# Kernel optimization log

Measured on AMD Instinct MI355X. Metric: run time of the kernel, lower is better.

## Reference

```python
import jax, jax.numpy as jnp
import numpy as np
from jax import lax

B, C, H, W = 4, 64, 256, 256
CH = C // 2  # attention hidden channels


def conv2d_same(x, w, b):
    # x: [B,Ci,H,W], w: [Co,Ci,kh,kw]
    y = lax.conv_general_dilated(x, w, (1, 1), 'SAME',
                                 dimension_numbers=('NCHW', 'OIHW', 'NCHW'))
    return y + b[None, :, None, None]


def conv1x1(x, w):
    # w: [Co,Ci]
    return jnp.einsum('oi,bihw->bohw', w, x)


def irnn_scan(x, w, b, axis, reverse):
    """Directional IRNN: h_t = relu(x_t + w_c * h_{t-1} + b_c), per channel.
    axis: 2 (rows/H) or 3 (cols/W). reverse=True scans from the far edge
    (e.g. bottom-to-top for 'up', right-to-left for 'left')."""
    xs = jnp.moveaxis(x, axis, 0)            # [L, B, C, rest]
    wb = w[None, :, None]                    # broadcast over [B, C, rest]
    bb = b[None, :, None]

    def step(h, xt):
        h = jax.nn.relu(xt + wb * h + bb)
        return h, h

    h0 = jnp.zeros_like(xs[0])
    _, ys = lax.scan(step, h0, xs, reverse=reverse)
    return jnp.moveaxis(ys, 0, axis)


def setup_inputs() -> dict:
    key = jax.random.key(0)
    ks = jax.random.split(key, 16)
    d = {}
    d['x'] = jax.random.normal(ks[0], (B, C, H, W), dtype=jnp.float32)
    # conv_in: 1x1, no bias
    d['w_in'] = jax.random.normal(ks[1], (C, C), dtype=jnp.float32) * 0.05
    # IRNN depthwise 1x1 weights (init alpha=1.0 in torch) + biases
    for i, name in enumerate(['up', 'right', 'down', 'left']):
        d['w_' + name] = jnp.ones((C,), dtype=jnp.float32)
        d['b_' + name] = jax.random.normal(ks[2 + i], (C,), dtype=jnp.float32) * 0.01
    # convD2: 1x1, 4C -> C, no bias
    d['wD2'] = jax.random.normal(ks[6], (C, 4 * C), dtype=jnp.float32) * 0.01
    # attention layers
    d['a1_w'] = jax.random.normal(ks[7], (CH, C, 3, 3), dtype=jnp.float32) * 0.05
    d['a1_b'] = jnp.zeros((CH,), dtype=jnp.float32)
    d['a2_w'] = jax.random.normal(ks[8], (CH, CH, 3, 3), dtype=jnp.float32) * 0.05
    d['a2_b'] = jnp.zeros((CH,), dtype=jnp.float32)
    d['a3_w'] = jax.random.normal(ks[9], (1, CH), dtype=jnp.float32) * 0.05
    d['a3_b'] = jnp.zeros((1,), dtype=jnp.float32)
    return d


def reference(x, w_in, w_up, b_up, w_right, b_right, w_down, b_down,
              w_left, b_left, wD2, a1_w, a1_b, a2_w, a2_b, a3_w, a3_b):
    out = conv1x1(x, w_in)
    # four directional spatial IRNN scans
    top_up = irnn_scan(out, w_up, b_up, axis=2, reverse=True)     # bottom->top
    top_right = irnn_scan(out, w_right, b_right, axis=3, reverse=False)  # left->right
    top_down = irnn_scan(out, w_down, b_down, axis=2, reverse=False)     # top->bottom
    top_left = irnn_scan(out, w_left, b_left, axis=3, reverse=True)      # right->left
    cat = jnp.concatenate([top_up, top_right, top_down, top_left], axis=1)  # [B,4C,H,W]
    out = jax.nn.relu(conv1x1(cat, wD2))
    # attention gate
    a = jax.nn.relu(conv2d_same(out, a1_w, a1_b))
    a = jax.nn.relu(conv2d_same(a, a2_w, a2_b))
    a = conv1x1(a, a3_w) + a3_b[None, :, None, None]
    weight = jax.nn.sigmoid(a)                # [B,1,H,W]
    return jax.nn.relu(x * weight)
```

## Files before the change

### kernel.cpp

```cpp
#include <hip/hip_runtime.h>
#include <hip/hip_bf16.h>

#define HWSZ  65536

typedef unsigned short ushort_t;
typedef unsigned int   uint_t;
typedef __attribute__((ext_vector_type(8))) _Float16 half8;
typedef __attribute__((ext_vector_type(2))) _Float16 half2v;
typedef __attribute__((ext_vector_type(4))) float f32x4;

static __device__ __forceinline__ void gl_lds16(const void* g, void* l) {
    __builtin_amdgcn_global_load_lds(
        (const __attribute__((address_space(1))) unsigned int*)g,
        (__attribute__((address_space(3))) unsigned int*)l, 16, 0, 0);
}

__global__ __launch_bounds__(256) void k1_mfma(
    const float* __restrict__ x, const float* __restrict__ w_in,
    _Float16* __restrict__ out0)
{
    __shared__ float xs[64][64];
    __shared__ _Float16 ah[64][72];
    __shared__ _Float16 al[64][72];
    int b   = blockIdx.x >> 10;
    int hw0 = (blockIdx.x & 1023) << 6;
    const float* xb = x + ((size_t)b * 64) * HWSZ + hw0;
    int wave = threadIdx.x >> 6, lane = threadIdx.x & 63;
    int n16 = lane & 15, quad = lane >> 4;

    for (int idx = threadIdx.x; idx < 1024; idx += 256) {
        int i = idx >> 4, p4 = (idx & 15) << 2;
        *(float4*)&xs[i][p4] = *(const float4*)(xb + (size_t)i * HWSZ + p4);
    }

    half8 Bh[2], Bl[2];
#pragma unroll
    for (int s = 0; s < 2; s++) {
        const float* wp = w_in + (wave * 16 + n16) * 64 + s * 32 + quad * 8;
#pragma unroll
        for (int j = 0; j < 8; j++) {
            float v = wp[j];
            _Float16 h = (_Float16)v;
            float r = v - (float)h;
            Bh[s][j] = h; Bl[s][j] = (_Float16)r;
        }
    }
    __syncthreads();

    {
        int px  = threadIdx.x & 63;
        int ic0 = (threadIdx.x >> 6) << 4;
        half8 h0, h1, l0, l1;
#pragma unroll
        for (int e = 0; e < 8; e++) {
            float v = xs[ic0 + e][px];
            _Float16 h = (_Float16)v;
            h0[e] = h; l0[e] = (_Float16)(v - (float)h);
        }
#pragma unroll
        for (int e = 0; e < 8; e++) {
            float v = xs[ic0 + 8 + e][px];
            _Float16 h = (_Float16)v;
            h1[e] = h; l1[e] = (_Float16)(v - (float)h);
        }
        *(half8*)&ah[px][ic0]     = h0;
        *(half8*)&ah[px][ic0 + 8] = h1;
        *(half8*)&al[px][ic0]     = l0;
        *(half8*)&al[px][ic0 + 8] = l1;
    }
    __syncthreads();

    f32x4 acc[4] = {};
#pragma unroll
    for (int j = 0; j < 4; j++) {
        int px = j * 16 + n16;
#pragma unroll
        for (int s = 0; s < 2; s++) {
            half8 Ah = *(const half8*)&ah[px][s * 32 + quad * 8];
            half8 Al = *(const half8*)&al[px][s * 32 + quad * 8];
            acc[j] = __builtin_amdgcn_mfma_f32_16x16x32_f16(Ah, Bh[s], acc[j], 0, 0, 0);
            acc[j] = __builtin_amdgcn_mfma_f32_16x16x32_f16(Al, Bh[s], acc[j], 0, 0, 0);
            acc[j] = __builtin_amdgcn_mfma_f32_16x16x32_f16(Ah, Bl[s], acc[j], 0, 0, 0);
        }
    }
    _Float16* ob = out0 + ((size_t)b * HWSZ + hw0) * 64 + wave * 16;
#pragma unroll
    for (int j = 0; j < 4; j++)
#pragma unroll
        for (int r = 0; r < 4; r++) {
            int px = j * 16 + quad * 4 + r;
            ob[(size_t)px * 64 + n16] = (_Float16)acc[j][r];
        }
}

__global__ __launch_bounds__(256) void k2_scan(
    const _Float16* __restrict__ out0,
    const float* __restrict__ w_up, const float* __restrict__ b_up,
    const float* __restrict__ w_rt, const float* __restrict__ b_rt,
    const float* __restrict__ w_dn, const float* __restrict__ b_dn,
    const float* __restrict__ w_lf, const float* __restrict__ b_lf,
    _Float16* __restrict__ cat)
{
    int c2 = threadIdx.x & 31;
    int q  = threadIdx.x >> 5;
    int dir = blockIdx.x >> 7;
    int bid = blockIdx.x & 127;
    int b = bid >> 5, g = bid & 31;
    int line = g * 8 + q;
    size_t base = (size_t)b * HWSZ;
    bool vert = dir < 2;
    bool rev  = dir & 1;

    const float *wp, *bp; int coff;
    if      (dir == 0) { wp = w_dn; bp = b_dn; coff = 128; }
    else if (dir == 1) { wp = w_up; bp = b_up; coff = 0;   }
    else if (dir == 2) { wp = w_rt; bp = b_rt; coff = 64;  }
    else               { wp = w_lf; bp = b_lf; coff = 192; }
    float w0v = wp[2 * c2], b0v = bp[2 * c2];
    float w1v = wp[2 * c2 + 1], b1v = bp[2 * c2 + 1];
    int coff2 = coff >> 1;

    const half2v* src = (const half2v*)out0;
    half2v* dst = (half2v*)cat;

    float h0 = 0.f, h1 = 0.f;
    for (int k0 = 0; k0 < 256; k0 += 16) {
        half2v v[16];
#pragma unroll
        for (int jx = 0; jx < 16; jx++) {
            int i = rev ? 255 - (k0 + jx) : (k0 + jx);
            size_t pix = vert ? (base + i * 256 + line) : (base + line * 256 + i);
            v[jx] = src[pix * 32 + c2];
        }
#pragma unroll
        for (int jx = 0; jx < 16; jx++) {
            int i = rev ? 255 - (k0 + jx) : (k0 + jx);
            size_t pix = vert ? (base + i * 256 + line) : (base + line * 256 + i);
            h0 = fmaxf(0.f, (float)v[jx][0] + w0v * h0 + b0v);
            h1 = fmaxf(0.f, (float)v[jx][1] + w1v * h1 + b1v);
            half2v o; o[0] = (_Float16)h0; o[1] = (_Float16)h1;
            dst[pix * 128 + coff2 + c2] = o;
        }
    }
}

__global__ __launch_bounds__(256) void packall(
    const float* __restrict__ wD2, const float* __restrict__ a1w,
    const float* __restrict__ a2w,
    _Float16* __restrict__ wf, _Float16* __restrict__ p1,
    _Float16* __restrict__ p2)
{
    int i = blockIdx.x * 256 + threadIdx.x;
    if (i < 16384) {
        wf[i] = (_Float16)wD2[i];
        return;
    }
    int k = i - 16384;
    if (k < 18432) {
        int j = k & 7, lane = (k >> 3) & 63, st = k >> 9;
        int s = st >> 1, t = st & 1;
        int oc = t * 16 + (lane & 15);
        int gk = s * 32 + (lane >> 4) * 8 + j;
        int dydx = gk >> 6, ic = gk & 63;
        p1[k] = (_Float16)a1w[((oc * 64 + ic) * 3 + dydx / 3) * 3 + dydx % 3];
    } else if (k < 27648) {
        int e = k - 18432;
        int j = e & 7, lane = (e >> 3) & 63, st = e >> 9;
        int s = st >> 1, t = st & 1;
        int oc = t * 16 + (lane & 15);
        int gk = s * 32 + (lane >> 4) * 8 + j;
        int dydx = gk >> 5, ic = gk & 31;
        p2[e] = (_Float16)a2w[((oc * 32 + ic) * 3 + dydx / 3) * 3 + dydx % 3];
    }
}

__global__ __launch_bounds__(256) void k3_mfma(
    const _Float16* __restrict__ cat, const _Float16* __restrict__ wf,
    _Float16* __restrict__ out3)
{
    __shared__ _Float16 As[64 * 256];
    int wave = threadIdx.x >> 6, lane = threadIdx.x & 63;
    int n16 = lane & 15, quad = lane >> 4;
    size_t p0 = (size_t)blockIdx.x * 64;

    half8 B[8];
#pragma unroll
    for (int s = 0; s < 8; s++)
        B[s] = *(const half8*)(wf + (size_t)(wave * 16 + n16) * 256 + s * 32 + quad * 8);

#pragma unroll
    for (int it = 0; it < 8; it++) {
        int px = wave * 16 + it * 2 + (lane >> 5);
        int pu = lane & 31;
        int lu = pu ^ (px & 7);
        const _Float16* gp = cat + ((p0 + px) << 8) + lu * 8;
        _Float16* lp = As + wave * 4096 + it * 512;
        gl_lds16(gp, lp);
    }
    __syncthreads();

    f32x4 acc[4] = {};
#pragma unroll
    for (int j = 0; j < 4; j++) {
        int px = j * 16 + n16;
        const _Float16* lrow = As + px * 256;
        int x7 = px & 7;
#pragma unroll
        for (int s = 0; s < 8; s++) {
            int phys = (s * 4 + quad) ^ x7;
            half8 a = *(const half8*)(lrow + phys * 8);
            acc[j] = __builtin_amdgcn_mfma_f32_16x16x32_f16(a, B[s], acc[j], 0, 0, 0);
        }
    }

#pragma unroll
    for (int j = 0; j < 4; j++)
#pragma unroll
        for (int r = 0; r < 4; r++) {
            size_t op = (p0 + j * 16 + quad * 4 + r) * 64 + wave * 16 + n16;
            out3[op] = (_Float16)fmaxf(acc[j][r], 0.f);
        }
}

template <int IC>
__global__ __launch_bounds__(256) void convmfma(
    const _Float16* __restrict__ in, const _Float16* __restrict__ pb,
    const float* __restrict__ bias, _Float16* __restrict__ oh)
{
    constexpr int UPX = IC / 8;
    constexpr int KST = IC / 32;
    constexpr int PPS = 64 / UPX;
    __shared__ _Float16 Ls[6 * 66 * IC];

    int wave = threadIdx.x >> 6, lane = threadIdx.x & 63;
    int n16 = lane & 15, quad = lane >> 4;
    int bid = blockIdx.x;
    int bb  = bid >> 8;
    int hh0 = ((bid >> 2) & 63) << 2;
    int w0  = (bid & 3) << 6;
    const _Float16* ib = in + (size_t)bb * HWSZ * IC;

#pragma unroll
    for (int it = 0; it < (6 * UPX) / 4; it++) {
        int q   = it * 4 + wave;
        int r   = q / UPX, seg = q % UPX;
        int gh  = hh0 - 1 + r;
        int pxr = seg * PPS + lane / UPX;
        int pu  = lane % UPX;
        int px_lin = r * 66 + 1 + pxr;
        int lu  = (UPX == 8) ? (pu ^ (px_lin & 7)) : pu;
        _Float16* lp = Ls + (size_t)(r * 66 + 1 + seg * PPS) * IC;
        if ((unsigned)gh < 256u) {
            const _Float16* gp = ib + ((size_t)(gh * 256 + w0 + pxr)) * IC + lu * 8;
            gl_lds16(gp, lp);
        } else {
            half8 z = {};
            *(half8*)(lp + (size_t)lane * 8) = z;
        }
    }
    if (threadIdx.x < 12 * UPX) {
        int pu = threadIdx.x % UPX;
        int ph = threadIdx.x / UPX;
        int r = ph >> 1, side = ph & 1;
        int col = side ? 65 : 0;
        int gh = hh0 - 1 + r;
        int gw = w0 - 1 + side * 65;
        int px_lin = r * 66 + col;
        int lu = (UPX == 8) ? (pu ^ (px_lin & 7)) : pu;
        half8 v = {};
        if ((unsigned)gh < 256u && (unsigned)gw < 256u)
            v = *(const half8*)(ib + ((size_t)(gh * 256 + gw)) * IC + lu * 8);
        *(half8*)(Ls + (size_t)px_lin * IC + pu * 8) = v;
    }
    __syncthreads();

    f32x4 acc[4][2] = {};
#pragma unroll
    for (int dydx = 0; dydx < 9; dydx++) {
        int dy = dydx / 3, dx = dydx % 3;
        int r_lds = wave + dy;
#pragma unroll
        for (int kst = 0; kst < KST; kst++) {
            int s = dydx * KST + kst;
            half8 B0 = *(const half8*)(pb + (size_t)((s * 2 + 0) * 64 + lane) * 8);
            half8 B1 = *(const half8*)(pb + (size_t)((s * 2 + 1) * 64 + lane) * 8);
            int u = kst * 4 + quad;
#pragma unroll
            for (int j = 0; j < 4; j++) {
                int px_lin = r_lds * 66 + j * 16 + n16 + dx;
                int phys = (UPX == 8) ? (u ^ (px_lin & 7)) : u;
                half8 A = *(const half8*)(Ls + (size_t)px_lin * IC + phys * 8);
                acc[j][0] = __builtin_amdgcn_mfma_f32_16x16x32_f16(A, B0, acc[j][0], 0, 0, 0);
                acc[j][1] = __builtin_amdgcn_mfma_f32_16x16x32_f16(A, B1, acc[j][1], 0, 0, 0);
            }
        }
    }

    int hh = hh0 + wave;
#pragma unroll
    for (int t = 0; t < 2; t++) {
        float bv = bias[t * 16 + n16];
#pragma unroll
        for (int j = 0; j < 4; j++)
#pragma unroll
            for (int r = 0; r < 4; r++) {
                int wp = w0 + j * 16 + quad * 4 + r;
                size_t op = ((size_t)bb * HWSZ + hh * 256 + wp) * 32 + t * 16 + n16;
                oh[op] = (_Float16)fmaxf(acc[j][t][r] + bv, 0.f);
            }
    }
}

__global__ __launch_bounds__(256) void k6g(
    const _Float16* __restrict__ a2, const float* __restrict__ a3w,
    const float* __restrict__ a3b, float* __restrict__ gbuf)
{
    int pix = blockIdx.x * 256 + threadIdx.x;
    const _Float16* ap = a2 + (size_t)pix * 32;
    half8 q0 = *(const half8*)(ap);
    half8 q1 = *(const half8*)(ap + 8);
    half8 q2 = *(const half8*)(ap + 16);
    half8 q3 = *(const half8*)(ap + 24);
    float s = a3b[0];
#pragma unroll
    for (int j = 0; j < 8; j++) {
        s += a3w[j]      * (float)q0[j];
        s += a3w[j + 8]  * (float)q1[j];
        s += a3w[j + 16] * (float)q2[j];
        s += a3w[j + 24] * (float)q3[j];
    }
    gbuf[pix] = 1.f / (1.f + __expf(-s));
}

__global__ __launch_bounds__(256) void k6b(
    const float* __restrict__ x, const float* __restrict__ gbuf,
    float* __restrict__ out)
{
    const float4* x4 = (const float4*)x;
    const float4* g4 = (const float4*)gbuf;
    float4* o4 = (float4*)out;
    size_t base = (size_t)blockIdx.x * 2048;
#pragma unroll
    for (int k = 0; k < 8; k++) {
        size_t e = base + k * 256 + threadIdx.x;
        int plane = (int)(e >> 14);
        int hw4   = (int)(e & 16383);
        int b     = plane >> 6;
        float4 xv = x4[e];
        float4 gv = g4[(size_t)b * 16384 + hw4];
        float4 ov;
        ov.x = fmaxf(0.f, xv.x * gv.x);
        ov.y = fmaxf(0.f, xv.y * gv.y);
        ov.z = fmaxf(0.f, xv.z * gv.z);
        ov.w = fmaxf(0.f, xv.w * gv.w);
        o4[e] = ov;
    }
}

extern "C" void kernel_launch(void* const* d_in, const int* in_sizes, int n_in,
                              void* d_out, int out_size, void* d_ws, size_t ws_size,
                              hipStream_t stream)
{
    const float* x     = (const float*)d_in[0];
    const float* w_in  = (const float*)d_in[1];
    const float* w_up  = (const float*)d_in[2];
    const float* b_up  = (const float*)d_in[3];
    const float* w_rt  = (const float*)d_in[4];
    const float* b_rt  = (const float*)d_in[5];
    const float* w_dn  = (const float*)d_in[6];
    const float* b_dn  = (const float*)d_in[7];
    const float* w_lf  = (const float*)d_in[8];
    const float* b_lf  = (const float*)d_in[9];
    const float* wD2   = (const float*)d_in[10];
    const float* a1w   = (const float*)d_in[11];
    const float* a1b   = (const float*)d_in[12];
    const float* a2w   = (const float*)d_in[13];
    const float* a2b   = (const float*)d_in[14];
    const float* a3w   = (const float*)d_in[15];
    const float* a3b   = (const float*)d_in[16];
    float* out = (float*)d_out;

    char* ws = (char*)d_ws;
    _Float16* out0 = (_Float16*)ws;
    _Float16* out3 = (_Float16*)ws;
    _Float16* wf16 = (_Float16*)(ws + (33ull << 20));
    _Float16* p1   = (_Float16*)(ws + (34ull << 20));
    _Float16* p2   = (_Float16*)(ws + (35ull << 20));
    float*    gbuf = (float*)   (ws + (36ull << 20));
    _Float16* cat  = (_Float16*)(ws + (64ull << 20));
    _Float16* a1   = (_Float16*)(ws + (64ull << 20));
    _Float16* a2   = (_Float16*)(ws + (80ull << 20));

    k1_mfma   <<<4096, 256, 0, stream>>>(x, w_in, out0);
    k2_scan   <<<512,  256, 0, stream>>>(out0, w_up, b_up, w_rt, b_rt,
                                         w_dn, b_dn, w_lf, b_lf, cat);
    packall   <<<172,  256, 0, stream>>>(wD2, a1w, a2w, wf16, p1, p2);
    k3_mfma   <<<4096, 256, 0, stream>>>(cat, wf16, out3);
    convmfma<64><<<1024, 256, 0, stream>>>(out3, p1, a1b, a1);
    convmfma<32><<<1024, 256, 0, stream>>>(a1, p2, a2b, a2);
    k6g       <<<1024, 256, 0, stream>>>(a2, a3w, a3b, gbuf);
    k6b       <<<2048, 256, 0, stream>>>(x, gbuf, out);
}
```

Baseline: 270.6 us.

## Split IRNN scans into two halves and fuse gate conv into second attention conv

The scan kernel now gives each line to two thread groups. One half runs the recurrence over the first 128 steps while the other prefetches the second 128 inputs into shared memory, then finishes the scan from the carried hidden state. This doubles the grid and shortens the serial latency chain spent on loads. Separately, the 1x1 gate projection and sigmoid are folded into the epilogue of the second 3x3 conv using cross-lane shuffles, which removes the a2 intermediate write/read and one kernel launch.

```diff
diff --git a/kernel.cpp b/kernel.cpp
--- a/kernel.cpp
+++ b/kernel.cpp
@@ -101,12 +101,15 @@
     const float* __restrict__ w_lf, const float* __restrict__ b_lf,
     _Float16* __restrict__ cat)
 {
-    int c2 = threadIdx.x & 31;
-    int q  = threadIdx.x >> 5;
-    int dir = blockIdx.x >> 7;
-    int bid = blockIdx.x & 127;
-    int b = bid >> 5, g = bid & 31;
-    int line = g * 8 + q;
+    __shared__ half2v ls[4][128][32];
+    __shared__ float hmid[4][32][2];
+    int c2   = threadIdx.x & 31;
+    int q    = (threadIdx.x >> 5) & 3;
+    int half = threadIdx.x >> 7;
+    int dir  = blockIdx.x >> 8;
+    int bid  = blockIdx.x & 255;
+    int b = bid >> 6, g = bid & 63;
+    int line = g * 4 + q;
     size_t base = (size_t)b * HWSZ;
     bool vert = dir < 2;
     bool rev  = dir & 1;
@@ -123,25 +126,52 @@
     const half2v* src = (const half2v*)out0;
     half2v* dst = (half2v*)cat;
 
-    float h0 = 0.f, h1 = 0.f;
-    for (int k0 = 0; k0 < 256; k0 += 16) {
-        half2v v[16];
-#pragma unroll
-        for (int jx = 0; jx < 16; jx++) {
-            int i = rev ? 255 - (k0 + jx) : (k0 + jx);
-            size_t pix = vert ? (base + i * 256 + line) : (base + line * 256 + i);
-            v[jx] = src[pix * 32 + c2];
-        }
-#pragma unroll
-        for (int jx = 0; jx < 16; jx++) {
-            int i = rev ? 255 - (k0 + jx) : (k0 + jx);
-            size_t pix = vert ? (base + i * 256 + line) : (base + line * 256 + i);
-            h0 = fmaxf(0.f, (float)v[jx][0] + w0v * h0 + b0v);
-            h1 = fmaxf(0.f, (float)v[jx][1] + w1v * h1 + b1v);
-            half2v o; o[0] = (_Float16)h0; o[1] = (_Float16)h1;
-            dst[pix * 128 + coff2 + c2] = o;
-        }
-    }
+#define PIXOF(k) (vert ? (base + (size_t)(rev ? 255 - (k) : (k)) * 256 + line) \
+                       : (base + line * 256 + (size_t)(rev ? 255 - (k) : (k))))
+
+    if (half == 0) {
+        float h0 = 0.f, h1 = 0.f;
+        for (int k0 = 0; k0 < 128; k0 += 16) {
+            half2v v[16];
+#pragma unroll
+            for (int jx = 0; jx < 16; jx++)
+                v[jx] = src[PIXOF(k0 + jx) * 32 + c2];
+#pragma unroll
+            for (int jx = 0; jx < 16; jx++) {
+                h0 = fmaxf(0.f, (float)v[jx][0] + w0v * h0 + b0v);
+                h1 = fmaxf(0.f, (float)v[jx][1] + w1v * h1 + b1v);
+                half2v o; o[0] = (_Float16)h0; o[1] = (_Float16)h1;
+                dst[PIXOF(k0 + jx) * 128 + coff2 + c2] = o;
+            }
+        }
+        hmid[q][c2][0] = h0; hmid[q][c2][1] = h1;
+    } else {
+        for (int k0 = 0; k0 < 128; k0 += 16) {
+            half2v v[16];
+#pragma unroll
+            for (int jx = 0; jx < 16; jx++)
+                v[jx] = src[PIXOF(128 + k0 + jx) * 32 + c2];
+#pragma unroll
+            for (int jx = 0; jx < 16; jx++)
+                ls[q][k0 + jx][c2] = v[jx];
+        }
+    }
+    __syncthreads();
+
+    if (half == 1) {
+        float h0 = hmid[q][c2][0], h1 = hmid[q][c2][1];
+        for (int k0 = 0; k0 < 128; k0 += 16) {
+#pragma unroll
+            for (int jx = 0; jx < 16; jx++) {
+                half2v v = ls[q][k0 + jx][c2];
+                h0 = fmaxf(0.f, (float)v[0] + w0v * h0 + b0v);
+                h1 = fmaxf(0.f, (float)v[1] + w1v * h1 + b1v);
+                half2v o; o[0] = (_Float16)h0; o[1] = (_Float16)h1;
+                dst[PIXOF(128 + k0 + jx) * 128 + coff2 + c2] = o;
+            }
+        }
+    }
+#undef PIXOF
 }
 
 __global__ __launch_bounds__(256) void packall(
@@ -222,10 +252,12 @@
         }
 }
 
-template <int IC>
+template <int IC, bool GATE>
 __global__ __launch_bounds__(256) void convmfma(
     const _Float16* __restrict__ in, const _Float16* __restrict__ pb,
-    const float* __restrict__ bias, _Float16* __restrict__ oh)
+    const float* __restrict__ bias, _Float16* __restrict__ oh,
+    const float* __restrict__ a3w, const float* __restrict__ a3b,
+    float* __restrict__ gbuf)
 {
     constexpr int UPX = IC / 8;
     constexpr int KST = IC / 32;
@@ -297,39 +329,40 @@
     }
 
     int hh = hh0 + wave;
-#pragma unroll
-    for (int t = 0; t < 2; t++) {
-        float bv = bias[t * 16 + n16];
+    if constexpr (GATE) {
+        float bv0 = bias[n16], bv1 = bias[16 + n16];
+        float aw0 = a3w[n16], aw1 = a3w[16 + n16];
+        float ab  = a3b[0];
 #pragma unroll
         for (int j = 0; j < 4; j++)
 #pragma unroll
             for (int r = 0; r < 4; r++) {
-                int wp = w0 + j * 16 + quad * 4 + r;
-                size_t op = ((size_t)bb * HWSZ + hh * 256 + wp) * 32 + t * 16 + n16;
-                oh[op] = (_Float16)fmaxf(acc[j][t][r] + bv, 0.f);
+                float r0 = fmaxf(acc[j][0][r] + bv0, 0.f);
+                float r1 = fmaxf(acc[j][1][r] + bv1, 0.f);
+                float sv = fmaf(aw0, r0, aw1 * r1);
+                sv += __shfl_xor(sv, 1, 16);
+                sv += __shfl_xor(sv, 2, 16);
+                sv += __shfl_xor(sv, 4, 16);
+                sv += __shfl_xor(sv, 8, 16);
+                if (n16 == 0) {
+                    float gg = 1.f / (1.f + __expf(-(sv + ab)));
+                    gbuf[(size_t)bb * HWSZ + hh * 256 + w0 + j * 16 + quad * 4 + r] = gg;
+                }
             }
-    }
-}
-
-__global__ __launch_bounds__(256) void k6g(
-    const _Float16* __restrict__ a2, const float* __restrict__ a3w,
-    const float* __restrict__ a3b, float* __restrict__ gbuf)
-{
-    int pix = blockIdx.x * 256 + threadIdx.x;
-    const _Float16* ap = a2 + (size_t)pix * 32;
-    half8 q0 = *(const half8*)(ap);
-    half8 q1 = *(const half8*)(ap + 8);
-    half8 q2 = *(const half8*)(ap + 16);
-    half8 q3 = *(const half8*)(ap + 24);
-    float s = a3b[0];
-#pragma unroll
-    for (int j = 0; j < 8; j++) {
-        s += a3w[j]      * (float)q0[j];
-        s += a3w[j + 8]  * (float)q1[j];
-        s += a3w[j + 16] * (float)q2[j];
-        s += a3w[j + 24] * (float)q3[j];
-    }
-    gbuf[pix] = 1.f / (1.f + __expf(-s));
+    } else {
+#pragma unroll
+        for (int t = 0; t < 2; t++) {
+            float bv = bias[t * 16 + n16];
+#pragma unroll
+            for (int j = 0; j < 4; j++)
+#pragma unroll
+                for (int r = 0; r < 4; r++) {
+                    int wp = w0 + j * 16 + quad * 4 + r;
+                    size_t op = ((size_t)bb * HWSZ + hh * 256 + wp) * 32 + t * 16 + n16;
+                    oh[op] = (_Float16)fmaxf(acc[j][t][r] + bv, 0.f);
+                }
+        }
+    }
 }
 
 __global__ __launch_bounds__(256) void k6b(
@@ -389,15 +422,15 @@
     float*    gbuf = (float*)   (ws + (36ull << 20));
     _Float16* cat  = (_Float16*)(ws + (64ull << 20));
     _Float16* a1   = (_Float16*)(ws + (64ull << 20));
-    _Float16* a2   = (_Float16*)(ws + (80ull << 20));
 
     k1_mfma   <<<4096, 256, 0, stream>>>(x, w_in, out0);
-    k2_scan   <<<512,  256, 0, stream>>>(out0, w_up, b_up, w_rt, b_rt,
+    k2_scan   <<<1024, 256, 0, stream>>>(out0, w_up, b_up, w_rt, b_rt,
                                          w_dn, b_dn, w_lf, b_lf, cat);
     packall   <<<172,  256, 0, stream>>>(wD2, a1w, a2w, wf16, p1, p2);
     k3_mfma   <<<4096, 256, 0, stream>>>(cat, wf16, out3);
-    convmfma<64><<<1024, 256, 0, stream>>>(out3, p1, a1b, a1);
-    convmfma<32><<<1024, 256, 0, stream>>>(a1, p2, a2b, a2);
-    k6g       <<<1024, 256, 0, stream>>>(a2, a3w, a3b, gbuf);
+    convmfma<64, false><<<1024, 256, 0, stream>>>(out3, p1, a1b, a1,
+                                                  nullptr, nullptr, nullptr);
+    convmfma<32, true> <<<1024, 256, 0, stream>>>(a1, p2, a2b, nullptr,
+                                                  a3w, a3b, gbuf);
     k6b       <<<2048, 256, 0, stream>>>(x, gbuf, out);
 }
```

Result: no change. 266.6 us (-1.5%).

## Fuse attention 1x1 gate into second conv and load conv_in operands directly

Applied to the files above, without the earlier changes.

The second 3x3 attention conv now computes the 1x1 projection to a single channel and the sigmoid in its epilogue, using a 16-lane shuffle reduction. This removes the a2 intermediate write/read and the separate gate kernel launch. Separately, the input 1x1 conv kernel drops its LDS staging and transpose, loading fp32 x values straight from global into registers per MFMA fragment. That removes two barriers and the LDS traffic, but the loads become strided per lane (one element per channel plane) and may coalesce worse.

```diff
diff --git a/kernel.cpp b/kernel.cpp
--- a/kernel.cpp
+++ b/kernel.cpp
@@ -19,20 +19,12 @@
     const float* __restrict__ x, const float* __restrict__ w_in,
     _Float16* __restrict__ out0)
 {
-    __shared__ float xs[64][64];
-    __shared__ _Float16 ah[64][72];
-    __shared__ _Float16 al[64][72];
     int b   = blockIdx.x >> 10;
     int hw0 = (blockIdx.x & 1023) << 6;
     const float* xb = x + ((size_t)b * 64) * HWSZ + hw0;
     int wave = threadIdx.x >> 6, lane = threadIdx.x & 63;
     int n16 = lane & 15, quad = lane >> 4;
 
-    for (int idx = threadIdx.x; idx < 1024; idx += 256) {
-        int i = idx >> 4, p4 = (idx & 15) << 2;
-        *(float4*)&xs[i][p4] = *(const float4*)(xb + (size_t)i * HWSZ + p4);
-    }
-
     half8 Bh[2], Bl[2];
 #pragma unroll
     for (int s = 0; s < 2; s++) {
@@ -45,39 +37,24 @@
             Bh[s][j] = h; Bl[s][j] = (_Float16)r;
         }
     }
-    __syncthreads();
-
-    {
-        int px  = threadIdx.x & 63;
-        int ic0 = (threadIdx.x >> 6) << 4;
-        half8 h0, h1, l0, l1;
-#pragma unroll
-        for (int e = 0; e < 8; e++) {
-            float v = xs[ic0 + e][px];
-            _Float16 h = (_Float16)v;
-            h0[e] = h; l0[e] = (_Float16)(v - (float)h);
-        }
-#pragma unroll
-        for (int e = 0; e < 8; e++) {
-            float v = xs[ic0 + 8 + e][px];
-            _Float16 h = (_Float16)v;
-            h1[e] = h; l1[e] = (_Float16)(v - (float)h);
-        }
-        *(half8*)&ah[px][ic0]     = h0;
-        *(half8*)&ah[px][ic0 + 8] = h1;
-        *(half8*)&al[px][ic0]     = l0;
-        *(half8*)&al[px][ic0 + 8] = l1;
-    }
-    __syncthreads();
 
     f32x4 acc[4] = {};
 #pragma unroll
     for (int j = 0; j < 4; j++) {
         int px = j * 16 + n16;
+        const float* ap = xb + px + (size_t)(quad * 8) * HWSZ;
 #pragma unroll
         for (int s = 0; s < 2; s++) {
-            half8 Ah = *(const half8*)&ah[px][s * 32 + quad * 8];
-            half8 Al = *(const half8*)&al[px][s * 32 + quad * 8];
+            float v[8];
+#pragma unroll
+            for (int jj = 0; jj < 8; jj++)
+                v[jj] = ap[(size_t)(s * 32 + jj) * HWSZ];
+            half8 Ah, Al;
+#pragma unroll
+            for (int jj = 0; jj < 8; jj++) {
+                _Float16 h = (_Float16)v[jj];
+                Ah[jj] = h; Al[jj] = (_Float16)(v[jj] - (float)h);
+            }
             acc[j] = __builtin_amdgcn_mfma_f32_16x16x32_f16(Ah, Bh[s], acc[j], 0, 0, 0);
             acc[j] = __builtin_amdgcn_mfma_f32_16x16x32_f16(Al, Bh[s], acc[j], 0, 0, 0);
             acc[j] = __builtin_amdgcn_mfma_f32_16x16x32_f16(Ah, Bl[s], acc[j], 0, 0, 0);
@@ -222,10 +199,12 @@
         }
 }
 
-template <int IC>
+template <int IC, bool GATE>
 __global__ __launch_bounds__(256) void convmfma(
     const _Float16* __restrict__ in, const _Float16* __restrict__ pb,
-    const float* __restrict__ bias, _Float16* __restrict__ oh)
+    const float* __restrict__ bias, _Float16* __restrict__ oh,
+    const float* __restrict__ a3w, const float* __restrict__ a3b,
+    float* __restrict__ gbuf)
 {
     constexpr int UPX = IC / 8;
     constexpr int KST = IC / 32;
@@ -297,39 +276,40 @@
     }
 
     int hh = hh0 + wave;
-#pragma unroll
-    for (int t = 0; t < 2; t++) {
-        float bv = bias[t * 16 + n16];
+    if constexpr (GATE) {
+        float bv0 = bias[n16], bv1 = bias[16 + n16];
+        float aw0 = a3w[n16], aw1 = a3w[16 + n16];
+        float ab  = a3b[0];
 #pragma unroll
         for (int j = 0; j < 4; j++)
 #pragma unroll
             for (int r = 0; r < 4; r++) {
-                int wp = w0 + j * 16 + quad * 4 + r;
-                size_t op = ((size_t)bb * HWSZ + hh * 256 + wp) * 32 + t * 16 + n16;
-                oh[op] = (_Float16)fmaxf(acc[j][t][r] + bv, 0.f);
+                float r0 = fmaxf(acc[j][0][r] + bv0, 0.f);
+                float r1 = fmaxf(acc[j][1][r] + bv1, 0.f);
+                float sv = fmaf(aw0, r0, aw1 * r1);
+                sv += __shfl_xor(sv, 1, 16);
+                sv += __shfl_xor(sv, 2, 16);
+                sv += __shfl_xor(sv, 4, 16);
+                sv += __shfl_xor(sv, 8, 16);
+                if (n16 == 0) {
+                    float gg = 1.f / (1.f + __expf(-(sv + ab)));
+                    gbuf[(size_t)bb * HWSZ + hh * 256 + w0 + j * 16 + quad * 4 + r] = gg;
+                }
             }
-    }
-}
-
-__global__ __launch_bounds__(256) void k6g(
-    const _Float16* __restrict__ a2, const float* __restrict__ a3w,
-    const float* __restrict__ a3b, float* __restrict__ gbuf)
-{
-    int pix = blockIdx.x * 256 + threadIdx.x;
-    const _Float16* ap = a2 + (size_t)pix * 32;
-    half8 q0 = *(const half8*)(ap);
-    half8 q1 = *(const half8*)(ap + 8);
-    half8 q2 = *(const half8*)(ap + 16);
-    half8 q3 = *(const half8*)(ap + 24);
-    float s = a3b[0];
-#pragma unroll
-    for (int j = 0; j < 8; j++) {
-        s += a3w[j]      * (float)q0[j];
-        s += a3w[j + 8]  * (float)q1[j];
-        s += a3w[j + 16] * (float)q2[j];
-        s += a3w[j + 24] * (float)q3[j];
-    }
-    gbuf[pix] = 1.f / (1.f + __expf(-s));
+    } else {
+#pragma unroll
+        for (int t = 0; t < 2; t++) {
+            float bv = bias[t * 16 + n16];
+#pragma unroll
+            for (int j = 0; j < 4; j++)
+#pragma unroll
+                for (int r = 0; r < 4; r++) {
+                    int wp = w0 + j * 16 + quad * 4 + r;
+                    size_t op = ((size_t)bb * HWSZ + hh * 256 + wp) * 32 + t * 16 + n16;
+                    oh[op] = (_Float16)fmaxf(acc[j][t][r] + bv, 0.f);
+                }
+        }
+    }
 }
 
 __global__ __launch_bounds__(256) void k6b(
@@ -389,15 +369,15 @@
     float*    gbuf = (float*)   (ws + (36ull << 20));
     _Float16* cat  = (_Float16*)(ws + (64ull << 20));
     _Float16* a1   = (_Float16*)(ws + (64ull << 20));
-    _Float16* a2   = (_Float16*)(ws + (80ull << 20));
 
     k1_mfma   <<<4096, 256, 0, stream>>>(x, w_in, out0);
     k2_scan   <<<512,  256, 0, stream>>>(out0, w_up, b_up, w_rt, b_rt,
                                          w_dn, b_dn, w_lf, b_lf, cat);
     packall   <<<172,  256, 0, stream>>>(wD2, a1w, a2w, wf16, p1, p2);
     k3_mfma   <<<4096, 256, 0, stream>>>(cat, wf16, out3);
-    convmfma<64><<<1024, 256, 0, stream>>>(out3, p1, a1b, a1);
-    convmfma<32><<<1024, 256, 0, stream>>>(a1, p2, a2b, a2);
-    k6g       <<<1024, 256, 0, stream>>>(a2, a3w, a3b, gbuf);
+    convmfma<64, false><<<1024, 256, 0, stream>>>(out3, p1, a1b, a1,
+                                                  nullptr, nullptr, nullptr);
+    convmfma<32, true> <<<1024, 256, 0, stream>>>(a1, p2, a2b, nullptr,
+                                                  a3w, a3b, gbuf);
     k6b       <<<2048, 256, 0, stream>>>(x, gbuf, out);
 }
```

Result: no change. 275.4 us (+1.7%).
